# Optimization experiments

Measured on AMD Instinct MI355X. Metric: run time of the kernel, lower is better.

## Reference

```python
import jax, jax.numpy as jnp
import numpy as np

N_NODES = 100000
N_EDGES = 6400000
IN_DIM = 10
HIDDEN = 16


def setup_inputs() -> dict:
    key = jax.random.key(0)
    k1, k2, k3, k4, k5 = jax.random.split(key, 5)
    x = jax.random.normal(k1, (N_NODES, IN_DIM), dtype=jnp.float32)
    edge_index = jax.random.randint(k2, (2, N_EDGES), 0, N_NODES, dtype=jnp.int64)
    W_l = jax.random.normal(k3, (IN_DIM, HIDDEN), dtype=jnp.float32) * (1.0 / np.sqrt(IN_DIM))
    b_l = jax.random.normal(k4, (HIDDEN,), dtype=jnp.float32) * 0.01
    W_r = jax.random.normal(k5, (IN_DIM, HIDDEN), dtype=jnp.float32) * (1.0 / np.sqrt(IN_DIM))
    return {"x": x, "edge_index": edge_index, "W_l": W_l, "b_l": b_l, "W_r": W_r}


def reference(x, edge_index, W_l, b_l, W_r):
    # PyG SAGEConv (aggr='mean', root_weight=True):
    #   out = lin_l(mean_{j in N(i)} x_j) + lin_r(x_i)
    n = x.shape[0]
    src, dst = edge_index[0], edge_index[1]
    msgs = x[src]                                   # [E, IN] gather
    summed = jax.ops.segment_sum(msgs, dst, num_segments=n)          # [N, IN]
    counts = jax.ops.segment_sum(jnp.ones((src.shape[0],), x.dtype), dst, num_segments=n)
    mean = summed / jnp.maximum(counts, 1.0)[:, None]                # [N, IN]
    out = mean @ W_l + b_l + x @ W_r                                  # [N, HIDDEN]
    return out
```

## Files before the change

### kernel.cpp

```cpp
#include <hip/hip_runtime.h>

#define N_NODES 100000
#define N_EDGES 6400000
#define IN_DIM 10
#define HIDDEN 16

#define BKT_SHIFT 8
#define BKT_NODES 256
#define NBKT 391
#define RBIN 38
#define EPB 10240
#define NB1 ((N_EDGES + EPB - 1) / EPB)
#define CAPB 18432
#define SPLIT 4
#define CHUNK ((CAPB + SPLIT - 1) / SPLIT)
#define PROW 11

__global__ __launch_bounds__(512) void bin_edges(const int* __restrict__ src,
                                                 const int* __restrict__ dst,
                                                 int* __restrict__ gcur,
                                                 unsigned* __restrict__ region) {
    __shared__ int lcur[NBKT];
    __shared__ unsigned lbin[NBKT * RBIN];
    for (int b = threadIdx.x; b < NBKT; b += 512) lcur[b] = 0;
    __syncthreads();

    int base = blockIdx.x * EPB;
    int end = min(base + EPB, N_EDGES);
    for (int i = base + (int)threadIdx.x; i < end; i += 512) {
        int s = src[i], d = dst[i];
        if ((unsigned)s >= N_NODES || (unsigned)d >= N_NODES) continue;
        unsigned pack = (unsigned)s | ((unsigned)(d & (BKT_NODES - 1)) << 17);
        int b = d >> BKT_SHIFT;
        int pos = atomicAdd(&lcur[b], 1);
        if (pos < RBIN) {
            lbin[b * RBIN + pos] = pack;
        } else {
            int g = atomicAdd(&gcur[b], 1);
            if (g < CAPB) region[(size_t)b * CAPB + g] = pack;
        }
    }
    __syncthreads();

    for (int b = threadIdx.x; b < NBKT; b += 512) {
        int f = min(lcur[b], RBIN);
        if (f > 0) {
            int g = atomicAdd(&gcur[b], f);
            unsigned* dp = region + (size_t)b * CAPB;
#pragma unroll 4
            for (int j = 0; j < f; ++j) {
                int gg = g + j;
                if (gg < CAPB) dp[gg] = lbin[b * RBIN + j];
            }
        }
    }
}

__global__ __launch_bounds__(512) void bucket_sort_partial(const float* __restrict__ x,
                                                           const int* __restrict__ gcur,
                                                           const unsigned* __restrict__ region,
                                                           float* __restrict__ partial) {
    __shared__ unsigned sorted[CHUNK];
    __shared__ int offs[BKT_NODES + 1];
    __shared__ int cursor[BKT_NODES];
    __shared__ int hist[BKT_NODES];

    int t = threadIdx.x;
    if (t < BKT_NODES) hist[t] = 0;
    __syncthreads();

    int b = blockIdx.x;
    int sp = blockIdx.y;
    int n = min(gcur[b], CAPB);
    int chunk = (n + SPLIT - 1) / SPLIT;
    int start = sp * chunk;
    int end = min(start + chunk, n);
    const unsigned* reg = region + (size_t)b * CAPB;

    for (int i = start + t; i < end; i += 512) {
        int local = (reg[i] >> 17) & (BKT_NODES - 1);
        atomicAdd(&hist[local], 1);
    }
    __syncthreads();

    if (t < 64) {
        int base4 = t * 4;
        int h0 = hist[base4], h1 = hist[base4 + 1], h2 = hist[base4 + 2], h3 = hist[base4 + 3];
        int sum4 = h0 + h1 + h2 + h3;
        int run = sum4;
#pragma unroll
        for (int o = 1; o < 64; o <<= 1) {
            int v = __shfl_up(run, o, 64);
            if (t >= o) run += v;
        }
        int excl = run - sum4;
        offs[base4] = excl;
        offs[base4 + 1] = excl + h0;
        offs[base4 + 2] = excl + h0 + h1;
        offs[base4 + 3] = excl + h0 + h1 + h2;
        cursor[base4] = excl;
        cursor[base4 + 1] = excl + h0;
        cursor[base4 + 2] = excl + h0 + h1;
        cursor[base4 + 3] = excl + h0 + h1 + h2;
        if (t == 63) offs[BKT_NODES] = excl + sum4;
    }
    __syncthreads();

    for (int i = start + t; i < end; i += 512) {
        unsigned e = reg[i];
        int local = (e >> 17) & (BKT_NODES - 1);
        int pos = atomicAdd(&cursor[local], 1);
        sorted[pos] = e & 0x1FFFF;
    }
    __syncthreads();

    int local = t >> 1;
    int half = t & 1;
    int s0 = offs[local];
    int s1 = offs[local + 1];
    float acc[IN_DIM];
#pragma unroll
    for (int k = 0; k < IN_DIM; ++k) acc[k] = 0.0f;
    float cnt = 0.0f;
    for (int i = s0 + half; i < s1; i += 2) {
        int s = sorted[i];
        const float2* xs = (const float2*)(x + (size_t)s * IN_DIM);
        float2 v0 = xs[0], v1 = xs[1], v2 = xs[2], v3 = xs[3], v4 = xs[4];
        acc[0] += v0.x; acc[1] += v0.y;
        acc[2] += v1.x; acc[3] += v1.y;
        acc[4] += v2.x; acc[5] += v2.y;
        acc[6] += v3.x; acc[7] += v3.y;
        acc[8] += v4.x; acc[9] += v4.y;
        cnt += 1.0f;
    }
#pragma unroll
    for (int k = 0; k < IN_DIM; ++k) acc[k] += __shfl_xor(acc[k], 1, 64);
    cnt += __shfl_xor(cnt, 1, 64);

    if (half == 0) {
        float* dp = partial + (((size_t)b * SPLIT + sp) * PROW) * BKT_NODES;
#pragma unroll
        for (int k = 0; k < IN_DIM; ++k) dp[(size_t)k * BKT_NODES + local] = acc[k];
        dp[(size_t)10 * BKT_NODES + local] = cnt;
    }
}

__global__ __launch_bounds__(512) void combine_out(const float* __restrict__ x,
                                                   const float* __restrict__ partial,
                                                   const float* __restrict__ W_l,
                                                   const float* __restrict__ b_l,
                                                   const float* __restrict__ W_r,
                                                   float* __restrict__ out) {
    __shared__ float sWl[IN_DIM * HIDDEN], sWr[IN_DIM * HIDDEN], sb[HIDDEN];
    int t = threadIdx.x;
    if (t < IN_DIM * HIDDEN) { sWl[t] = W_l[t]; sWr[t] = W_r[t]; }
    if (t < HIDDEN) sb[t] = b_l[t];
    __syncthreads();

    int node = blockIdx.x * 512 + t;
    if (node >= N_NODES) return;
    int b = node >> BKT_SHIFT;
    int local = node & (BKT_NODES - 1);

    float s[PROW];
#pragma unroll
    for (int k = 0; k < PROW; ++k) s[k] = 0.0f;
#pragma unroll
    for (int sp = 0; sp < SPLIT; ++sp) {
        const float* pp = partial + (((size_t)b * SPLIT + sp) * PROW) * BKT_NODES + local;
#pragma unroll
        for (int k = 0; k < PROW; ++k) s[k] += pp[(size_t)k * BKT_NODES];
    }

    float inv = 1.0f / fmaxf(s[10], 1.0f);
    const float* xp = x + (size_t)node * IN_DIM;
    float m[IN_DIM], xr[IN_DIM];
#pragma unroll
    for (int k = 0; k < IN_DIM; ++k) { m[k] = s[k] * inv; xr[k] = xp[k]; }

    float o[HIDDEN];
#pragma unroll
    for (int h = 0; h < HIDDEN; ++h) o[h] = sb[h];
#pragma unroll
    for (int k = 0; k < IN_DIM; ++k) {
#pragma unroll
        for (int h = 0; h < HIDDEN; ++h)
            o[h] += m[k] * sWl[k * HIDDEN + h] + xr[k] * sWr[k * HIDDEN + h];
    }
    float4* op = (float4*)(out + (size_t)node * HIDDEN);
    op[0] = make_float4(o[0], o[1], o[2], o[3]);
    op[1] = make_float4(o[4], o[5], o[6], o[7]);
    op[2] = make_float4(o[8], o[9], o[10], o[11]);
    op[3] = make_float4(o[12], o[13], o[14], o[15]);
}

__global__ void sage_scatter_fb(const float* __restrict__ x, const int* __restrict__ src,
                                const int* __restrict__ dst, float* __restrict__ summed,
                                float* __restrict__ counts) {
    int e = blockIdx.x * blockDim.x + threadIdx.x;
    if (e >= N_EDGES) return;
    int s = src[e], d = dst[e];
    if ((unsigned)s >= N_NODES || (unsigned)d >= N_NODES) return;
    const float* xs = x + (size_t)s * IN_DIM;
    float* sm = summed + (size_t)d * IN_DIM;
#pragma unroll
    for (int k = 0; k < IN_DIM; ++k) atomicAdd(&sm[k], xs[k]);
    atomicAdd(&counts[d], 1.0f);
}

__global__ void sage_out_fb(const float* __restrict__ x, const float* __restrict__ summed,
                            const float* __restrict__ counts, const float* __restrict__ W_l,
                            const float* __restrict__ b_l, const float* __restrict__ W_r,
                            float* __restrict__ out) {
    __shared__ float sWl[IN_DIM * HIDDEN], sWr[IN_DIM * HIDDEN], sb[HIDDEN];
    int t = threadIdx.x;
    if (t < IN_DIM * HIDDEN) { sWl[t] = W_l[t]; sWr[t] = W_r[t]; }
    if (t < HIDDEN) sb[t] = b_l[t];
    __syncthreads();
    int tid = blockIdx.x * blockDim.x + t;
    if (tid >= N_NODES * HIDDEN) return;
    int node = tid >> 4, h = tid & (HIDDEN - 1);
    float inv = 1.0f / fmaxf(counts[node], 1.0f);
    const float* sm = summed + (size_t)node * IN_DIM;
    const float* xr = x + (size_t)node * IN_DIM;
    float acc = sb[h];
#pragma unroll
    for (int k = 0; k < IN_DIM; ++k)
        acc += sm[k] * inv * sWl[k * HIDDEN + h] + xr[k] * sWr[k * HIDDEN + h];
    out[tid] = acc;
}

extern "C" void kernel_launch(void* const* d_in, const int* in_sizes, int n_in,
                              void* d_out, int out_size, void* d_ws, size_t ws_size,
                              hipStream_t stream) {
    const float* x   = (const float*)d_in[0];
    const int*   ei  = (const int*)d_in[1];
    const float* W_l = (const float*)d_in[2];
    const float* b_l = (const float*)d_in[3];
    const float* W_r = (const float*)d_in[4];
    float* out = (float*)d_out;
    const int* src = ei;
    const int* dst = ei + N_EDGES;

    const size_t region_off  = 4096;
    const size_t region_sz   = (size_t)NBKT * CAPB * 4;
    const size_t partial_off = region_off + region_sz;
    const size_t partial_sz  = (size_t)NBKT * SPLIT * PROW * BKT_NODES * 4;
    const size_t need = partial_off + partial_sz;

    if (ws_size >= need) {
        int* gcur = (int*)d_ws;
        unsigned* region = (unsigned*)((char*)d_ws + region_off);
        float* partial = (float*)((char*)d_ws + partial_off);

        hipMemsetAsync(gcur, 0, NBKT * sizeof(int), stream);

        bin_edges<<<NB1, 512, 0, stream>>>(src, dst, gcur, region);
        dim3 g2(NBKT, SPLIT);
        bucket_sort_partial<<<g2, 512, 0, stream>>>(x, gcur, region, partial);
        combine_out<<<(N_NODES + 511) / 512, 512, 0, stream>>>(x, partial, W_l, b_l, W_r, out);
    } else {
        float* summed = (float*)d_ws;
        float* counts = summed + (size_t)N_NODES * IN_DIM;
        hipMemsetAsync(d_ws, 0, (size_t)(N_NODES * IN_DIM + N_NODES) * sizeof(float), stream);
        int threads = 256;
        int eblocks = (N_EDGES + threads - 1) / threads;
        sage_scatter_fb<<<eblocks, threads, 0, stream>>>(x, src, dst, summed, counts);
        int oblocks = (N_NODES * HIDDEN + threads - 1) / threads;
        sage_out_fb<<<oblocks, threads, 0, stream>>>(x, summed, counts, W_l, b_l, W_r, out);
    }
}
```

Baseline: 230.7 us.

## Gather bf16-packed node features and fuse combine into sort kernel

The bin kernel now also converts x to bf16 in a padded 16-wide layout, and the gather loop reads the packed rows (one 16-byte and one 4-byte load) instead of five float2 loads, to cut gather bandwidth. The separate combine kernel is removed: the last split block per bucket, found by an atomic done counter, computes the output projection. Region entries are also cached in registers between the histogram and scatter passes to avoid re-reading them. This trades accuracy (bf16 rounding of neighbour features) and adds fence and atomic overhead in exchange for less memory traffic and one fewer launch.

```diff
diff --git a/kernel.cpp b/kernel.cpp
--- a/kernel.cpp
+++ b/kernel.cpp
@@ -14,15 +14,32 @@
 #define CAPB 18432
 #define SPLIT 4
 #define CHUNK ((CAPB + SPLIT - 1) / SPLIT)
+#define RPT (CHUNK / 512)
 #define PROW 11
-
-__global__ __launch_bounds__(512) void bin_edges(const int* __restrict__ src,
-                                                 const int* __restrict__ dst,
-                                                 int* __restrict__ gcur,
-                                                 unsigned* __restrict__ region) {
+#define XELEMS (N_NODES * IN_DIM)
+#define XE_PER_BLK ((XELEMS + NB1 - 1) / NB1)
+
+__device__ __forceinline__ float bf_lo(unsigned u) { return __uint_as_float(u << 16); }
+__device__ __forceinline__ float bf_hi(unsigned u) { return __uint_as_float(u & 0xffff0000u); }
+
+__global__ __launch_bounds__(512) void bin_edges_xpack(const int* __restrict__ src,
+                                                       const int* __restrict__ dst,
+                                                       const float* __restrict__ x,
+                                                       int* __restrict__ gcur,
+                                                       unsigned* __restrict__ region,
+                                                       unsigned short* __restrict__ xp) {
     __shared__ int lcur[NBKT];
     __shared__ unsigned lbin[NBKT * RBIN];
     for (int b = threadIdx.x; b < NBKT; b += 512) lcur[b] = 0;
+
+    int xbase = blockIdx.x * XE_PER_BLK;
+    int xend = min(xbase + XE_PER_BLK, XELEMS);
+    for (int e = xbase + (int)threadIdx.x; e < xend; e += 512) {
+        int row = e / 10;
+        int k = e - row * 10;
+        unsigned bits = __float_as_uint(x[e]);
+        xp[(size_t)row * 16 + k] = (unsigned short)((bits + 0x8000u) >> 16);
+    }
     __syncthreads();
 
     int base = blockIdx.x * EPB;
@@ -56,17 +73,27 @@
     }
 }
 
-__global__ __launch_bounds__(512) void bucket_sort_partial(const float* __restrict__ x,
-                                                           const int* __restrict__ gcur,
-                                                           const unsigned* __restrict__ region,
-                                                           float* __restrict__ partial) {
+__global__ __launch_bounds__(512) void sort_partial_combine(const unsigned short* __restrict__ xp,
+                                                            const float* __restrict__ x,
+                                                            const int* __restrict__ gcur,
+                                                            const unsigned* __restrict__ region,
+                                                            float* __restrict__ partial,
+                                                            int* __restrict__ done,
+                                                            const float* __restrict__ W_l,
+                                                            const float* __restrict__ b_l,
+                                                            const float* __restrict__ W_r,
+                                                            float* __restrict__ out) {
     __shared__ unsigned sorted[CHUNK];
     __shared__ int offs[BKT_NODES + 1];
     __shared__ int cursor[BKT_NODES];
     __shared__ int hist[BKT_NODES];
+    __shared__ float sWl[IN_DIM * HIDDEN], sWr[IN_DIM * HIDDEN], sb[HIDDEN];
+    __shared__ int s_prev;
 
     int t = threadIdx.x;
     if (t < BKT_NODES) hist[t] = 0;
+    if (t < IN_DIM * HIDDEN) { sWl[t] = W_l[t]; sWr[t] = W_r[t]; }
+    if (t < HIDDEN) sb[t] = b_l[t];
     __syncthreads();
 
     int b = blockIdx.x;
@@ -77,9 +104,12 @@
     int end = min(start + chunk, n);
     const unsigned* reg = region + (size_t)b * CAPB;
 
+    unsigned rcache[RPT];
+    int nr = 0;
     for (int i = start + t; i < end; i += 512) {
-        int local = (reg[i] >> 17) & (BKT_NODES - 1);
-        atomicAdd(&hist[local], 1);
+        unsigned e = reg[i];
+        rcache[nr++] = e;
+        atomicAdd(&hist[(e >> 17) & (BKT_NODES - 1)], 1);
     }
     __syncthreads();
 
@@ -106,8 +136,8 @@
     }
     __syncthreads();
 
-    for (int i = start + t; i < end; i += 512) {
-        unsigned e = reg[i];
+    for (int j = 0; j < nr; ++j) {
+        unsigned e = rcache[j];
         int local = (e >> 17) & (BKT_NODES - 1);
         int pos = atomicAdd(&cursor[local], 1);
         sorted[pos] = e & 0x1FFFF;
@@ -124,13 +154,14 @@
     float cnt = 0.0f;
     for (int i = s0 + half; i < s1; i += 2) {
         int s = sorted[i];
-        const float2* xs = (const float2*)(x + (size_t)s * IN_DIM);
-        float2 v0 = xs[0], v1 = xs[1], v2 = xs[2], v3 = xs[3], v4 = xs[4];
-        acc[0] += v0.x; acc[1] += v0.y;
-        acc[2] += v1.x; acc[3] += v1.y;
-        acc[4] += v2.x; acc[5] += v2.y;
-        acc[6] += v3.x; acc[7] += v3.y;
-        acc[8] += v4.x; acc[9] += v4.y;
+        const unsigned* px = (const unsigned*)(xp + (size_t)s * 16);
+        uint4 p = *((const uint4*)px);
+        unsigned q = px[4];
+        acc[0] += bf_lo(p.x); acc[1] += bf_hi(p.x);
+        acc[2] += bf_lo(p.y); acc[3] += bf_hi(p.y);
+        acc[4] += bf_lo(p.z); acc[5] += bf_hi(p.z);
+        acc[6] += bf_lo(p.w); acc[7] += bf_hi(p.w);
+        acc[8] += bf_lo(q);   acc[9] += bf_hi(q);
         cnt += 1.0f;
     }
 #pragma unroll
@@ -143,55 +174,46 @@
         for (int k = 0; k < IN_DIM; ++k) dp[(size_t)k * BKT_NODES + local] = acc[k];
         dp[(size_t)10 * BKT_NODES + local] = cnt;
     }
-}
-
-__global__ __launch_bounds__(512) void combine_out(const float* __restrict__ x,
-                                                   const float* __restrict__ partial,
-                                                   const float* __restrict__ W_l,
-                                                   const float* __restrict__ b_l,
-                                                   const float* __restrict__ W_r,
-                                                   float* __restrict__ out) {
-    __shared__ float sWl[IN_DIM * HIDDEN], sWr[IN_DIM * HIDDEN], sb[HIDDEN];
-    int t = threadIdx.x;
-    if (t < IN_DIM * HIDDEN) { sWl[t] = W_l[t]; sWr[t] = W_r[t]; }
-    if (t < HIDDEN) sb[t] = b_l[t];
-    __syncthreads();
-
-    int node = blockIdx.x * 512 + t;
-    if (node >= N_NODES) return;
-    int b = node >> BKT_SHIFT;
-    int local = node & (BKT_NODES - 1);
-
-    float s[PROW];
-#pragma unroll
-    for (int k = 0; k < PROW; ++k) s[k] = 0.0f;
-#pragma unroll
-    for (int sp = 0; sp < SPLIT; ++sp) {
-        const float* pp = partial + (((size_t)b * SPLIT + sp) * PROW) * BKT_NODES + local;
-#pragma unroll
-        for (int k = 0; k < PROW; ++k) s[k] += pp[(size_t)k * BKT_NODES];
-    }
-
-    float inv = 1.0f / fmaxf(s[10], 1.0f);
-    const float* xp = x + (size_t)node * IN_DIM;
-    float m[IN_DIM], xr[IN_DIM];
-#pragma unroll
-    for (int k = 0; k < IN_DIM; ++k) { m[k] = s[k] * inv; xr[k] = xp[k]; }
-
-    float o[HIDDEN];
-#pragma unroll
-    for (int h = 0; h < HIDDEN; ++h) o[h] = sb[h];
-#pragma unroll
-    for (int k = 0; k < IN_DIM; ++k) {
-#pragma unroll
-        for (int h = 0; h < HIDDEN; ++h)
-            o[h] += m[k] * sWl[k * HIDDEN + h] + xr[k] * sWr[k * HIDDEN + h];
-    }
-    float4* op = (float4*)(out + (size_t)node * HIDDEN);
-    op[0] = make_float4(o[0], o[1], o[2], o[3]);
-    op[1] = make_float4(o[4], o[5], o[6], o[7]);
-    op[2] = make_float4(o[8], o[9], o[10], o[11]);
-    op[3] = make_float4(o[12], o[13], o[14], o[15]);
+
+    __threadfence();
+    __syncthreads();
+    if (t == 0) s_prev = atomicAdd(&done[b], 1);
+    __syncthreads();
+    if (s_prev == SPLIT - 1) {
+        __threadfence();
+        if (t < BKT_NODES) {
+            int node = b * BKT_NODES + t;
+            if (node < N_NODES) {
+                float s[PROW];
+#pragma unroll
+                for (int k = 0; k < PROW; ++k) s[k] = 0.0f;
+#pragma unroll
+                for (int sp2 = 0; sp2 < SPLIT; ++sp2) {
+                    const float* pp = partial + (((size_t)b * SPLIT + sp2) * PROW) * BKT_NODES + t;
+#pragma unroll
+                    for (int k = 0; k < PROW; ++k) s[k] += pp[(size_t)k * BKT_NODES];
+                }
+                float inv = 1.0f / fmaxf(s[10], 1.0f);
+                const float* xr = x + (size_t)node * IN_DIM;
+                float o[HIDDEN];
+#pragma unroll
+                for (int h = 0; h < HIDDEN; ++h) o[h] = sb[h];
+#pragma unroll
+                for (int k = 0; k < IN_DIM; ++k) {
+                    float m = s[k] * inv;
+                    float xk = xr[k];
+#pragma unroll
+                    for (int h = 0; h < HIDDEN; ++h)
+                        o[h] += m * sWl[k * HIDDEN + h] + xk * sWr[k * HIDDEN + h];
+                }
+                float4* op = (float4*)(out + (size_t)node * HIDDEN);
+                op[0] = make_float4(o[0], o[1], o[2], o[3]);
+                op[1] = make_float4(o[4], o[5], o[6], o[7]);
+                op[2] = make_float4(o[8], o[9], o[10], o[11]);
+                op[3] = make_float4(o[12], o[13], o[14], o[15]);
+            }
+        }
+    }
 }
 
 __global__ void sage_scatter_fb(const float* __restrict__ x, const int* __restrict__ src,
@@ -246,19 +268,23 @@
     const size_t region_sz   = (size_t)NBKT * CAPB * 4;
     const size_t partial_off = region_off + region_sz;
     const size_t partial_sz  = (size_t)NBKT * SPLIT * PROW * BKT_NODES * 4;
-    const size_t need = partial_off + partial_sz;
+    const size_t xp_off      = partial_off + partial_sz;
+    const size_t xp_sz       = (size_t)N_NODES * 16 * 2;
+    const size_t need = xp_off + xp_sz;
 
     if (ws_size >= need) {
         int* gcur = (int*)d_ws;
+        int* done = (int*)((char*)d_ws + 2048);
         unsigned* region = (unsigned*)((char*)d_ws + region_off);
         float* partial = (float*)((char*)d_ws + partial_off);
-
-        hipMemsetAsync(gcur, 0, NBKT * sizeof(int), stream);
-
-        bin_edges<<<NB1, 512, 0, stream>>>(src, dst, gcur, region);
+        unsigned short* xp = (unsigned short*)((char*)d_ws + xp_off);
+
+        hipMemsetAsync(d_ws, 0, 4096, stream);
+
+        bin_edges_xpack<<<NB1, 512, 0, stream>>>(src, dst, x, gcur, region, xp);
         dim3 g2(NBKT, SPLIT);
-        bucket_sort_partial<<<g2, 512, 0, stream>>>(x, gcur, region, partial);
-        combine_out<<<(N_NODES + 511) / 512, 512, 0, stream>>>(x, partial, W_l, b_l, W_r, out);
+        sort_partial_combine<<<g2, 512, 0, stream>>>(xp, x, gcur, region, partial, done,
+                                                     W_l, b_l, W_r, out);
     } else {
         float* summed = (float*)d_ws;
         float* counts = summed + (size_t)N_NODES * IN_DIM;
```

Result: slower. 581.7 us (+152.1%).
